# Kernel optimization log

Hardware: AMD Instinct MI355X
Metric: run time of the kernel (lower is better)

Reference implementation:

```python
import jax, jax.numpy as jnp
import numpy as np

B, Hm, Wm, Dm = 1, 32, 32, 32
N = Hm * Wm * Dm
C = 128
HEADS, DH = 8, 16
G = 32
L = 2
OUT = 1


def _ln(x, g, b):
    mu = jnp.mean(x, -1, keepdims=True)
    var = jnp.mean((x - mu) ** 2, -1, keepdims=True)
    return (x - mu) * jax.lax.rsqrt(var + 1e-5) * g + b


def setup_inputs() -> dict:
    key = jax.random.key(0)
    ks = iter(jax.random.split(key, 64))
    def nrm(shape, s=0.02):
        return jax.random.normal(next(ks), shape, jnp.float32) * s
    return {
        "x": jax.random.normal(next(ks), (B, N, 3), jnp.float32),
        "fx": jax.random.normal(next(ks), (B, N, 1), jnp.float32),
        "pre_w1": nrm((4, 2 * C)), "pre_b1": jnp.zeros((2 * C,), jnp.float32),
        "pre_w2": nrm((2 * C, C)), "pre_b2": jnp.zeros((C,), jnp.float32),
        "placeholder": jax.random.uniform(next(ks), (C,), jnp.float32) / C,
        "ln1_g": jnp.ones((L, C), jnp.float32), "ln1_b": jnp.zeros((L, C), jnp.float32),
        "convx_w": nrm((L, C, C, 3, 3, 3)), "convx_b": jnp.zeros((L, C), jnp.float32),
        "convfx_w": nrm((L, C, C, 3, 3, 3)), "convfx_b": jnp.zeros((L, C), jnp.float32),
        "slice_w": nrm((L, DH, G), 0.1), "slice_b": jnp.zeros((L, G), jnp.float32),
        "temperature": jnp.full((L, 1, HEADS, 1, 1), 0.5, jnp.float32),
        "wq": nrm((L, DH, DH), 0.1), "wk": nrm((L, DH, DH), 0.1), "wv": nrm((L, DH, DH), 0.1),
        "wo": nrm((L, HEADS * DH, C)), "bo": jnp.zeros((L, C), jnp.float32),
        "ln2_g": jnp.ones((L, C), jnp.float32), "ln2_b": jnp.zeros((L, C), jnp.float32),
        "mlp_w1": nrm((L, C, C)), "mlp_b1": jnp.zeros((L, C), jnp.float32),
        "mlp_w2": nrm((L, C, C)), "mlp_b2": jnp.zeros((L, C), jnp.float32),
        "ln3_g": jnp.ones((C,), jnp.float32), "ln3_b": jnp.zeros((C,), jnp.float32),
        "out_w": nrm((C, OUT)), "out_b": jnp.zeros((OUT,), jnp.float32),
    }


def _conv3d(x, w, b):
    # x: [B,C,H,W,D], w: [O,I,3,3,3], SAME padding (kernel//2) as torch Conv3d
    y = jax.lax.conv_general_dilated(x, w, (1, 1, 1), "SAME",
                                     dimension_numbers=("NCDHW", "OIDHW", "NCDHW"))
    return y + b[None, :, None, None, None]


def _physics_attn(z, cw_x, cb_x, cw_fx, cb_fx, sw, sb, temp, wq, wk, wv, wo, bo):
    # z: [B, N, C] -> structured mesh conv projections -> slice attention
    xg = z.reshape(B, Hm, Wm, Dm, C).transpose(0, 4, 1, 2, 3)  # [B,C,H,W,D]

    def split_heads(t):  # [B,I,H,W,D] -> [B,heads,N,dh]
        return t.transpose(0, 2, 3, 4, 1).reshape(B, N, HEADS, DH).transpose(0, 2, 1, 3)

    x_mid = split_heads(_conv3d(xg, cw_x, cb_x))
    fx_mid = split_heads(_conv3d(xg, cw_fx, cb_fx))
    # slice assignment weights: [B,heads,N,G], temperature-scaled softmax
    slice_logits = (x_mid @ sw + sb) / temp
    swt = jax.nn.softmax(slice_logits, axis=-1)
    norm = jnp.sum(swt, axis=2)  # [B,heads,G]
    tok = jnp.einsum("bhnc,bhng->bhgc", fx_mid, swt) / (norm + 1e-5)[..., None]
    q, k, v = tok @ wq, tok @ wk, tok @ wv  # [B,heads,G,dh]
    attn = jax.nn.softmax((q @ k.transpose(0, 1, 3, 2)) * (DH ** -0.5), axis=-1)
    ot = attn @ v  # [B,heads,G,dh]
    out = jnp.einsum("bhgc,bhng->bhnc", ot, swt)  # de-slice back to tokens
    out = out.transpose(0, 2, 1, 3).reshape(B, N, HEADS * DH)
    return out @ wo + bo


def reference(x, fx, pre_w1, pre_b1, pre_w2, pre_b2, placeholder,
              ln1_g, ln1_b, convx_w, convx_b, convfx_w, convfx_b,
              slice_w, slice_b, temperature, wq, wk, wv, wo, bo,
              ln2_g, ln2_b, mlp_w1, mlp_b1, mlp_w2, mlp_b2,
              ln3_g, ln3_b, out_w, out_b):
    h = jnp.concatenate([x, fx], axis=-1)  # [B,N,space+fun]
    z = jax.nn.gelu(h @ pre_w1 + pre_b1, approximate=False) @ pre_w2 + pre_b2 + placeholder
    for l in range(L):
        zn = _ln(z, ln1_g[l], ln1_b[l])
        z = _physics_attn(zn, convx_w[l], convx_b[l], convfx_w[l], convfx_b[l],
                          slice_w[l], slice_b[l], temperature[l],
                          wq[l], wk[l], wv[l], wo[l], bo[l]) + z
        zn = _ln(z, ln2_g[l], ln2_b[l])
        z = jax.nn.gelu(zn @ mlp_w1[l] + mlp_b1[l], approximate=False) @ mlp_w2[l] + mlp_b2[l] + z
    return _ln(z, ln3_g, ln3_b) @ out_w + out_b
```

## Files before the change

kernel.cpp:

```cpp
#include <hip/hip_runtime.h>
#include <hip/hip_bf16.h>

#define DEV __device__ __forceinline__

constexpr int N   = 32768;
constexpr int TOTAL_IN = 2038481;

constexpr int OFF_X        = 0;
constexpr int OFF_FX       = 98304;
constexpr int OFF_PRE_W1   = 131072;
constexpr int OFF_PRE_B1   = 132096;
constexpr int OFF_PRE_W2   = 132352;
constexpr int OFF_PRE_B2   = 165120;
constexpr int OFF_PLACE    = 165248;
constexpr int OFF_LN1_G    = 165376;
constexpr int OFF_LN1_B    = 165632;
constexpr int OFF_CONVX_W  = 165888;
constexpr int OFF_CONVX_B  = 1050624;
constexpr int OFF_CONVFX_W = 1050880;
constexpr int OFF_CONVFX_B = 1935616;
constexpr int OFF_SLICE_W  = 1935872;
constexpr int OFF_SLICE_B  = 1936896;
constexpr int OFF_TEMP     = 1936960;
constexpr int OFF_WQ       = 1936976;
constexpr int OFF_WK       = 1937488;
constexpr int OFF_WV       = 1938000;
constexpr int OFF_WO       = 1938512;
constexpr int OFF_BO       = 1971280;
constexpr int OFF_LN2_G    = 1971536;
constexpr int OFF_LN2_B    = 1971792;
constexpr int OFF_MLP_W1   = 1972048;
constexpr int OFF_MLP_B1   = 2004816;
constexpr int OFF_MLP_W2   = 2005072;
constexpr int OFF_MLP_B2   = 2037840;
constexpr int OFF_LN3_G    = 2038096;
constexpr int OFF_LN3_B    = 2038224;
constexpr int OFF_OUT_W    = 2038352;
constexpr int OFF_OUT_B    = 2038480;

__device__ __constant__ int d_PRE[32] = {
  0, 98304, 131072, 132096, 132352, 165120, 165248, 165376, 165632,
  165888, 1050624, 1050880, 1935616, 1935872, 1936896, 1936960, 1936976,
  1937488, 1938000, 1938512, 1971280, 1971536, 1971792, 1972048, 2004816,
  2005072, 2037840, 2038096, 2038224, 2038352, 2038480, 2038481
};

constexpr size_t F_IN   = 16;
constexpr size_t F_WT   = 2038512;
constexpr size_t F_Z    = F_WT   + 1769472;
constexpr size_t F_ZN   = F_Z    + 4194304;
constexpr size_t F_CONV = F_ZN   + 4194304;
constexpr size_t F_SWT  = F_CONV + 8388608;
constexpr size_t F_TOKP = F_SWT  + 8388608;
constexpr size_t F_TOK2 = F_TOKP + 1114112;
constexpr size_t F_WP   = F_TOK2 + 34816;
constexpr size_t F_ZERO = F_WP   + 65536;
constexpr size_t F_END  = F_ZERO + 64;

struct InPtrs { const void* p[31]; };

typedef short short8v  __attribute__((ext_vector_type(8)));
typedef float float4v  __attribute__((ext_vector_type(4)));
#define MFMA16(A,B,C) __builtin_amdgcn_mfma_f32_16x16x32_bf16(A,B,C,0,0,0)

typedef const __attribute__((address_space(1))) void* gas_p;
typedef __attribute__((address_space(3))) void* las_p;

DEV float geluf(float x) { return 0.5f * x * (1.0f + erff(x * 0.70710678118654752f)); }
DEV short f2bs(float x) { union { __hip_bfloat16 h; short s; } c; c.h = __float2bfloat16(x); return c.s; }
DEV float bs2f(short s) { union { unsigned u; float f; } c; c.u = ((unsigned)(unsigned short)s) << 16; return c.f; }

__global__ void k_setup(InPtrs ptrs, float* __restrict__ ws,
                        short* __restrict__ wtf, short* __restrict__ wp) {
  __shared__ short wl[13952];
  const bool isbf = (*(const unsigned*)ptrs.p[15] == 0x3F003F00u);
  int b = blockIdx.x, tid = threadIdx.x;
  if (b < 512) {
    if (b == 0 && tid < 64) ws[F_ZERO + tid] = 0.f;
    int stride = 512 * 256;
    for (int e = b * 256 + tid; e < TOTAL_IN; e += stride) {
      if ((e >= OFF_CONVX_W && e < OFF_CONVX_B) || (e >= OFF_CONVFX_W && e < OFF_CONVFX_B)) continue;
      int lo = 0, hi = 30;
#pragma unroll
      for (int it = 0; it < 5; ++it) {
        int mid = (lo + hi + 1) >> 1;
        if (e >= d_PRE[mid]) lo = mid; else hi = mid - 1;
      }
      int loc = e - d_PRE[lo];
      float v;
      if (isbf) {
        unsigned short u = ((const unsigned short*)ptrs.p[lo])[loc];
        v = __uint_as_float(((unsigned)u) << 16);
      } else {
        v = ((const float*)ptrs.p[lo])[loc];
      }
      ws[F_IN + e] = v;
    }
  } else if (b < 640) {
    int idx = b - 512;
    int layer = idx >> 6, rem = idx & 63;
    int icb = rem >> 4, ntile = rem & 15;
    for (int i = tid; i < 13824; i += 256) {
      int oc_r = i / 864, off = i - oc_r * 864;
      int oc = ntile * 16 + oc_r;
      const void* cw = (oc < 128) ? ptrs.p[9] : ptrs.p[11];
      size_t base = ((size_t)(layer * 128 + (oc & 127)) * 128 + icb * 32) * 27 + off;
      wl[oc_r * 872 + off] = isbf ? (short)((const unsigned short*)cw)[base]
                                  : f2bs(((const float*)cw)[base]);
    }
    __syncthreads();
    int wv = tid >> 6, lane = tid & 63;
    int m = lane & 15, q = lane >> 4;
    for (int tg = 0; tg < 7; ++tg) {
      int tap = tg * 4 + wv;
      if (tap < 27) {
        short8v out;
#pragma unroll
        for (int j = 0; j < 8; ++j) out[j] = wl[m * 872 + (q * 8 + j) * 27 + tap];
        size_t f = ((size_t)((layer * 108 + icb * 27 + tap) * 16 + ntile)) * 64 + lane;
        *(short8v*)(wtf + f * 8) = out;
      }
    }
  } else {
    int f = (b - 640) * 256 + tid;
    int lane = f & 63;
    int t = f >> 6;
    const void* srcb; size_t soff; int kt, nt;
    if (t < 64) { srcb = ptrs.p[4]; soff = 0; kt = t >> 3; nt = t & 7; }
    else {
      int r = t - 64, l = r / 96, r2 = r - l * 96;
      int which = r2 >> 5, idx2 = r2 & 31;
      kt = idx2 >> 3; nt = idx2 & 7;
      srcb = (which == 0 ? ptrs.p[23] : (which == 1 ? ptrs.p[25] : ptrs.p[19]));
      soff = (size_t)l * 16384;
    }
    int k0 = kt * 32 + (lane >> 4) * 8;
    int n = nt * 16 + (lane & 15);
    size_t base = soff + (size_t)k0 * 128 + n;
    short8v out;
    if (isbf) {
      const unsigned short* src = (const unsigned short*)srcb + base;
#pragma unroll
      for (int j = 0; j < 8; ++j) out[j] = (short)src[(size_t)j * 128];
    } else {
      const float* src = (const float*)srcb + base;
#pragma unroll
      for (int j = 0; j < 8; ++j) out[j] = f2bs(src[(size_t)j * 128]);
    }
    *(short8v*)(wp + (size_t)f * 8) = out;
  }
}

__global__ __launch_bounds__(256)
void k_prenet(const float* __restrict__ ip, const short* __restrict__ wp,
              float* __restrict__ z, short* __restrict__ znb) {
  __shared__ float w1s[1024], b1s[256], cvec[128], g1s[128], be1s[128];
  __shared__ float xv[64][4];
  __shared__ __align__(16) short ts[64 * 264];
  int tid = threadIdx.x;
  int wv = tid >> 6, lane = tid & 63;
  int m = lane & 15, q = lane >> 4;
  int n0 = blockIdx.x * 64;
  for (int i = tid; i < 1024; i += 256) w1s[i] = ip[OFF_PRE_W1 + i];
  b1s[tid] = ip[OFF_PRE_B1 + tid];
  if (tid < 128) {
    cvec[tid] = ip[OFF_PRE_B2 + tid] + ip[OFF_PLACE + tid];
    g1s[tid]  = ip[OFF_LN1_G + tid];
    be1s[tid] = ip[OFF_LN1_B + tid];
  }
  if (tid < 64) {
    xv[tid][0] = ip[OFF_X + (n0 + tid) * 3 + 0];
    xv[tid][1] = ip[OFF_X + (n0 + tid) * 3 + 1];
    xv[tid][2] = ip[OFF_X + (n0 + tid) * 3 + 2];
    xv[tid][3] = ip[OFF_FX + n0 + tid];
  }
  __syncthreads();
  {
    float w0 = w1s[tid], wA = w1s[256 + tid], wB = w1s[512 + tid], wC = w1s[768 + tid];
    float bb = b1s[tid];
    for (int t = 0; t < 64; ++t) {
      float hv = bb + xv[t][0] * w0 + xv[t][1] * wA + xv[t][2] * wB + xv[t][3] * wC;
      ts[t * 264 + tid] = f2bs(geluf(hv));
    }
  }
  __syncthreads();
  const short8v* pwf = (const short8v*)wp;
  float4v acc[8];
#pragma unroll
  for (int nt = 0; nt < 8; ++nt) acc[nt] = (float4v){0.f, 0.f, 0.f, 0.f};
  for (int kt = 0; kt < 8; ++kt) {
    short8v A = *(const short8v*)(ts + (wv * 16 + m) * 264 + kt * 32 + q * 8);
#pragma unroll
    for (int nt = 0; nt < 8; ++nt)
      acc[nt] = MFMA16(A, pwf[(kt * 8 + nt) * 64 + lane], acc[nt]);
  }
  float vz[8][4];
#pragma unroll
  for (int nt = 0; nt < 8; ++nt) {
    int col = nt * 16 + m;
#pragma unroll
    for (int r = 0; r < 4; ++r) {
      vz[nt][r] = acc[nt][r] + cvec[col];
      z[(size_t)(n0 + wv * 16 + q * 4 + r) * 128 + col] = vz[nt][r];
    }
  }
#pragma unroll
  for (int r = 0; r < 4; ++r) {
    float s1 = 0.f, s2 = 0.f;
#pragma unroll
    for (int nt = 0; nt < 8; ++nt) { float v = vz[nt][r]; s1 += v; s2 += v * v; }
#pragma unroll
    for (int off = 1; off < 16; off <<= 1) { s1 += __shfl_xor(s1, off); s2 += __shfl_xor(s2, off); }
    float mu = s1 * (1.0f / 128.0f);
    float var = s2 * (1.0f / 128.0f) - mu * mu;
    float rst = 1.0f / sqrtf(var + 1e-5f);
    size_t rowb = (size_t)(n0 + wv * 16 + q * 4 + r) * 128;
#pragma unroll
    for (int nt = 0; nt < 8; ++nt) {
      int col = nt * 16 + m;
      znb[rowb + col] = f2bs((vz[nt][r] - mu) * rst * g1s[col] + be1s[col]);
    }
  }
}

__global__ __launch_bounds__(256)
void k_conv(const float* __restrict__ ip, const short* __restrict__ znb,
            const short* __restrict__ wtf, short* __restrict__ cvb,
            const float* __restrict__ zerof, int layer) {
  __shared__ __align__(16) short halo[26624];
  int tid = threadIdx.x;
  int wv = tid >> 6, lane = tid & 63;
  int m = lane & 15, q = lane >> 4;
  int n0 = blockIdx.x * 64;
  int h = n0 >> 10, w0 = (n0 >> 5) & 31;
  float bias_r[4];
#pragma unroll
  for (int nt = 0; nt < 4; ++nt) {
    int oc = (wv * 4 + nt) * 16 + m;
    bias_r[nt] = (oc < 128) ? ip[OFF_CONVX_B + layer * 128 + oc]
                            : ip[OFF_CONVFX_B + layer * 128 + (oc - 128)];
  }
  float4v acc[4][4];
#pragma unroll
  for (int a = 0; a < 4; ++a)
#pragma unroll
    for (int b = 0; b < 4; ++b) acc[a][b] = (float4v){0.f, 0.f, 0.f, 0.f};

  const short8v* wf = (const short8v*)wtf + (size_t)layer * 110592 + (wv * 4) * 64 + lane;
  short8v bc0 = wf[0], bc1 = wf[64], bc2 = wf[128], bc3 = wf[192];

  auto stage = [&](int icb, short* dst) {
    for (int g = wv; g < 26; g += 4) {
      int c = g * 64 + lane;
      int pr = c >> 2, qq = c & 3;
      int line = pr / 34, dpos = pr - line * 34;
      int hh2 = h + (line >> 2) - 1, ww2 = w0 + (line & 3) - 1, dd2 = dpos - 1;
      bool ok = (pr < 408) && ((unsigned)hh2 < 32u) && ((unsigned)ww2 < 32u) && ((unsigned)dd2 < 32u);
      int tok = (hh2 << 10) + (ww2 << 5) + dd2;
      const void* src = ok ? (const void*)(znb + (size_t)tok * 128 + icb * 32 + qq * 8)
                           : (const void*)zerof;
      __builtin_amdgcn_global_load_lds((gas_p)src, (las_p)(dst + g * 512), 16, 0, 0);
    }
  };

  stage(0, halo);
  __syncthreads();

  int tap = 0, icb = 0;
  for (int kt = 0; kt < 108; ++kt) {
    if (tap == 0 && icb < 3)
      stage(icb + 1, halo + ((icb + 1) & 1) * 13312);
    int ktn = (kt + 1 < 108) ? kt + 1 : kt;
    const short8v* wn = wf + (size_t)ktn * 1024;
    short8v bn0 = wn[0], bn1 = wn[64], bn2 = wn[128], bn3 = wn[192];

    int ta = tap / 9, rem = tap - ta * 9, tb = rem / 3, tc = rem - tb * 3;
    const short* hp = halo + (icb & 1) * 13312 + ((ta * 4 + tb) * 34 + tc + m) * 32 + q * 8;
    short8v A0 = *(const short8v*)(hp);
    short8v A1 = *(const short8v*)(hp + 512);
    short8v A2 = *(const short8v*)(hp + 1088);
    short8v A3 = *(const short8v*)(hp + 1600);

    acc[0][0] = MFMA16(A0, bc0, acc[0][0]);
    acc[1][0] = MFMA16(A1, bc0, acc[1][0]);
    acc[2][0] = MFMA16(A2, bc0, acc[2][0]);
    acc[3][0] = MFMA16(A3, bc0, acc[3][0]);
    acc[0][1] = MFMA16(A0, bc1, acc[0][1]);
    acc[1][1] = MFMA16(A1, bc1, acc[1][1]);
    acc[2][1] = MFMA16(A2, bc1, acc[2][1]);
    acc[3][1] = MFMA16(A3, bc1, acc[3][1]);
    acc[0][2] = MFMA16(A0, bc2, acc[0][2]);
    acc[1][2] = MFMA16(A1, bc2, acc[1][2]);
    acc[2][2] = MFMA16(A2, bc2, acc[2][2]);
    acc[3][2] = MFMA16(A3, bc2, acc[3][2]);
    acc[0][3] = MFMA16(A0, bc3, acc[0][3]);
    acc[1][3] = MFMA16(A1, bc3, acc[1][3]);
    acc[2][3] = MFMA16(A2, bc3, acc[2][3]);
    acc[3][3] = MFMA16(A3, bc3, acc[3][3]);

    bc0 = bn0; bc1 = bn1; bc2 = bn2; bc3 = bn3;
    if (++tap == 27) {
      tap = 0; ++icb;
      __syncthreads();
    }
  }
#pragma unroll
  for (int mt = 0; mt < 4; ++mt) {
    short* cp = cvb + (size_t)(n0 + mt * 16 + q * 4) * 256 + (wv * 4) * 16 + m;
#pragma unroll
    for (int nt = 0; nt < 4; ++nt) {
#pragma unroll
      for (int r = 0; r < 4; ++r)
        cp[(size_t)r * 256 + nt * 16] = f2bs(acc[mt][nt][r] + bias_r[nt]);
    }
  }
}

__global__ __launch_bounds__(256)
void k_slice(const float* __restrict__ ip, const short* __restrict__ cvb,
             short* __restrict__ swtb, float* __restrict__ tokp, int layer) {
  __shared__ float sws[512], sbs[32], its[8];
  __shared__ float swl[32 * 257];
  __shared__ __align__(16) short fxl[32 * 132];
  int tid = threadIdx.x;
  for (int i = tid; i < 512; i += 256) sws[i] = ip[OFF_SLICE_W + layer * 512 + i];
  if (tid < 32) sbs[tid] = ip[OFF_SLICE_B + layer * 32 + tid];
  if (tid < 8)  its[tid] = 1.0f / ip[OFF_TEMP + layer * 8 + tid];
  float4 ta0 = make_float4(0,0,0,0), ta1 = ta0, ta2 = ta0, ta3 = ta0;
  float np = 0.f;
  for (int s = 0; s < 4; ++s) {
    int tbase = blockIdx.x * 128 + s * 32;
    __syncthreads();
    for (int i = tid; i < 512; i += 256) {
      int t = i >> 4, c8 = (i & 15) * 8;
      *(short8v*)(fxl + t * 132 + c8) = *(const short8v*)(cvb + (size_t)(tbase + t) * 256 + 128 + c8);
    }
    {
      int t = tid >> 3, hh = tid & 7;
      float xm[16];
      short8v x0 = *(const short8v*)(cvb + (size_t)(tbase + t) * 256 + hh * 16);
      short8v x1 = *(const short8v*)(cvb + (size_t)(tbase + t) * 256 + hh * 16 + 8);
#pragma unroll
      for (int j = 0; j < 8; ++j) { xm[j] = bs2f(x0[j]); xm[8 + j] = bs2f(x1[j]); }
      float lg[32];
      float itv = its[hh];
#pragma unroll
      for (int g = 0; g < 32; ++g) {
        float sacc = sbs[g];
#pragma unroll
        for (int j = 0; j < 16; ++j) sacc += xm[j] * sws[j * 32 + g];
        lg[g] = sacc * itv;
      }
      float mx = -1e30f;
#pragma unroll
      for (int g = 0; g < 32; ++g) mx = fmaxf(mx, lg[g]);
      float sum = 0.f;
#pragma unroll
      for (int g = 0; g < 32; ++g) { lg[g] = expf(lg[g] - mx); sum += lg[g]; }
      float inv = 1.0f / sum;
#pragma unroll
      for (int g = 0; g < 32; ++g) {
        lg[g] *= inv;
        swl[t * 257 + hh * 32 + g] = lg[g];
      }
#pragma unroll
      for (int qq = 0; qq < 4; ++qq) {
        short8v pk;
#pragma unroll
        for (int j = 0; j < 8; ++j) pk[j] = f2bs(lg[qq * 8 + j]);
        *(short8v*)(swtb + (size_t)(tbase + t) * 256 + hh * 32 + qq * 8) = pk;
      }
    }
    __syncthreads();
    {
      int ah = tid >> 5, ag = tid & 31;
      for (int t2 = 0; t2 < 32; ++t2) {
        float sv = swl[t2 * 257 + ah * 32 + ag];
        np += sv;
        short8v f0 = *(const short8v*)(fxl + t2 * 132 + ah * 16);
        short8v f1 = *(const short8v*)(fxl + t2 * 132 + ah * 16 + 8);
        ta0.x += sv * bs2f(f0[0]); ta0.y += sv * bs2f(f0[1]); ta0.z += sv * bs2f(f0[2]); ta0.w += sv * bs2f(f0[3]);
        ta1.x += sv * bs2f(f0[4]); ta1.y += sv * bs2f(f0[5]); ta1.z += sv * bs2f(f0[6]); ta1.w += sv * bs2f(f0[7]);
        ta2.x += sv * bs2f(f1[0]); ta2.y += sv * bs2f(f1[1]); ta2.z += sv * bs2f(f1[2]); ta2.w += sv * bs2f(f1[3]);
        ta3.x += sv * bs2f(f1[4]); ta3.y += sv * bs2f(f1[5]); ta3.z += sv * bs2f(f1[6]); ta3.w += sv * bs2f(f1[7]);
      }
    }
  }
  int ah = tid >> 5, ag = tid & 31;
  size_t base = (size_t)blockIdx.x * 4352 + (size_t)(ah * 32 + ag) * 16;
  *(float4*)&tokp[base + 0]  = ta0;
  *(float4*)&tokp[base + 4]  = ta1;
  *(float4*)&tokp[base + 8]  = ta2;
  *(float4*)&tokp[base + 12] = ta3;
  tokp[(size_t)blockIdx.x * 4352 + 4096 + ah * 32 + ag] = np;
}

__global__ void k_tokred1(const float* __restrict__ tokp, float* __restrict__ tok2) {
  int ogrp = blockIdx.x % 17, bgrp = blockIdx.x / 17;
  int o = ogrp * 256 + threadIdx.x;
  float s = 0.f;
  int b0 = bgrp * 32;
#pragma unroll 8
  for (int b = b0; b < b0 + 32; ++b) s += tokp[(size_t)b * 4352 + o];
  tok2[(size_t)bgrp * 4352 + o] = s;
}

__global__ __launch_bounds__(256)
void k_fused(const float* __restrict__ ip, const short* __restrict__ swtb,
             const float* __restrict__ tok2, const short* __restrict__ wp,
             float* __restrict__ z, short* __restrict__ znb,
             void* __restrict__ dout, const void* __restrict__ tempraw, int layer) {
  __shared__ __align__(16) char smem[64512];
  short* otb = (short*)smem;
  float* bia = (float*)(smem + 8192);
  float* trs = (float*)(smem + 12288);
  short* znt = (short*)(smem + 12288);
  float* kk  = (float*)(smem + 29696);
  short* al  = (short*)(smem + 29696);
  float* vvs = (float*)(smem + 47104);
  float* bol = bia, *b1s = bia + 128, *b2s = bia + 256, *g2s = bia + 384;
  float* be2s = bia + 512, *lng = bia + 640, *lnb = bia + 768, *ows = bia + 896;
  int tid = threadIdx.x;
  int wv = tid >> 6, lane = tid & 63;
  int m = lane & 15, q = lane >> 4;
  int n0 = blockIdx.x * 64;
  if (tid < 128) {
    bol[tid]  = ip[OFF_BO + layer * 128 + tid];
    b1s[tid]  = ip[OFF_MLP_B1 + layer * 128 + tid];
    b2s[tid]  = ip[OFF_MLP_B2 + layer * 128 + tid];
    g2s[tid]  = ip[OFF_LN2_G + layer * 128 + tid];
    be2s[tid] = ip[OFF_LN2_B + layer * 128 + tid];
    if (layer == 0) {
      lng[tid] = ip[OFF_LN1_G + 128 + tid];
      lnb[tid] = ip[OFF_LN1_B + 128 + tid];
      ows[tid] = 0.f;
    } else {
      lng[tid] = ip[OFF_LN3_G + tid];
      lnb[tid] = ip[OFF_LN3_B + tid];
      ows[tid] = ip[OFF_OUT_W + tid];
    }
  }
  for (int i = tid; i < 4352; i += 256) {
    float s = 0.f;
#pragma unroll
    for (int b = 0; b < 8; ++b) s += tok2[(size_t)b * 4352 + i];
    trs[i] = s;
  }
  __syncthreads();
  float qv[16];
  {
    const float* wqp = ip + OFF_WQ + layer * 256;
    const float* wkp = ip + OFF_WK + layer * 256;
    const float* wvp = ip + OFF_WV + layer * 256;
    float inv = 1.0f / (trs[4096 + tid] + 1e-5f);
    float t[16];
#pragma unroll
    for (int c = 0; c < 16; ++c) t[c] = trs[tid * 16 + c] * inv;
#pragma unroll
    for (int c = 0; c < 16; ++c) {
      float aq = 0.f, ak = 0.f, av = 0.f;
#pragma unroll
      for (int j = 0; j < 16; ++j) {
        float tv = t[j];
        aq += tv * wqp[j * 16 + c];
        ak += tv * wkp[j * 16 + c];
        av += tv * wvp[j * 16 + c];
      }
      qv[c] = aq;
      kk[tid * 17 + c] = ak;
      vvs[tid * 17 + c] = av;
    }
  }
  __syncthreads();
  {
    int hh = tid >> 5, g = tid & 31;
    float sc[32];
    float mx = -1e30f;
#pragma unroll
    for (int g2 = 0; g2 < 32; ++g2) {
      float s = 0.f;
#pragma unroll
      for (int c = 0; c < 16; ++c) s += qv[c] * kk[(hh * 32 + g2) * 17 + c];
      s *= 0.25f;
      sc[g2] = s; mx = fmaxf(mx, s);
    }
    float sum = 0.f;
#pragma unroll
    for (int g2 = 0; g2 < 32; ++g2) { sc[g2] = expf(sc[g2] - mx); sum += sc[g2]; }
    float inv2 = 1.0f / sum;
    float o[16];
#pragma unroll
    for (int c = 0; c < 16; ++c) o[c] = 0.f;
#pragma unroll
    for (int g2 = 0; g2 < 32; ++g2) {
      float p = sc[g2] * inv2;
#pragma unroll
      for (int c = 0; c < 16; ++c) o[c] += p * vvs[(hh * 32 + g2) * 17 + c];
    }
#pragma unroll
    for (int dh = 0; dh < 16; ++dh)
      otb[hh * 512 + (((g >> 3) * 16 + dh) << 3) + (g & 7)] = f2bs(o[dh]);
  }
  __syncthreads();
  float4v accd[8];
#pragma unroll
  for (int h = 0; h < 8; ++h) accd[h] = (float4v){0.f, 0.f, 0.f, 0.f};
#pragma unroll
  for (int h = 0; h < 8; ++h) {
    short8v A = *(const short8v*)(swtb + (size_t)(n0 + wv * 16 + m) * 256 + h * 32 + q * 8);
    accd[h] = MFMA16(A, *(const short8v*)(otb + h * 512 + lane * 8), accd[h]);
  }
  __syncthreads();
#pragma unroll
  for (int h = 0; h < 8; ++h)
#pragma unroll
    for (int r = 0; r < 4; ++r)
      al[(wv * 16 + q * 4 + r) * 136 + h * 16 + m] = f2bs(accd[h][r]);
  __syncthreads();
  const short8v* wof = (const short8v*)(wp + (size_t)(128 + 96 * layer) * 512);
  float4v a2[8];
#pragma unroll
  for (int nt = 0; nt < 8; ++nt) a2[nt] = (float4v){0.f, 0.f, 0.f, 0.f};
  for (int kt = 0; kt < 4; ++kt) {
    short8v A = *(const short8v*)(al + (wv * 16 + m) * 136 + kt * 32 + q * 8);
#pragma unroll
    for (int nt = 0; nt < 8; ++nt)
      a2[nt] = MFMA16(A, wof[(kt * 8 + nt) * 64 + lane], a2[nt]);
  }
  float vmid[8][4];
#pragma unroll
  for (int nt = 0; nt < 8; ++nt) {
    int col = nt * 16 + m;
#pragma unroll
    for (int r = 0; r < 4; ++r)
      vmid[nt][r] = z[(size_t)(n0 + wv * 16 + q * 4 + r) * 128 + col] + a2[nt][r] + bol[col];
  }
#pragma unroll
  for (int r = 0; r < 4; ++r) {
    float s1 = 0.f, s2 = 0.f;
#pragma unroll
    for (int nt = 0; nt < 8; ++nt) { float v = vmid[nt][r]; s1 += v; s2 += v * v; }
#pragma unroll
    for (int off = 1; off < 16; off <<= 1) { s1 += __shfl_xor(s1, off); s2 += __shfl_xor(s2, off); }
    float mu = s1 * (1.0f / 128.0f);
    float var = s2 * (1.0f / 128.0f) - mu * mu;
    float rst = 1.0f / sqrtf(var + 1e-5f);
#pragma unroll
    for (int nt = 0; nt < 8; ++nt) {
      int col = nt * 16 + m;
      znt[(wv * 16 + q * 4 + r) * 136 + col] = f2bs((vmid[nt][r] - mu) * rst * g2s[col] + be2s[col]);
    }
  }
  __syncthreads();
  const short8v* w1f = (const short8v*)(wp + (size_t)(64 + 96 * layer) * 512);
  const short8v* w2f = (const short8v*)(wp + (size_t)(96 + 96 * layer) * 512);
  float4v acc[8];
#pragma unroll
  for (int nt = 0; nt < 8; ++nt) acc[nt] = (float4v){0.f, 0.f, 0.f, 0.f};
  for (int kt = 0; kt < 4; ++kt) {
    short8v A = *(const short8v*)(znt + (wv * 16 + m) * 136 + kt * 32 + q * 8);
#pragma unroll
    for (int nt = 0; nt < 8; ++nt)
      acc[nt] = MFMA16(A, w1f[(kt * 8 + nt) * 64 + lane], acc[nt]);
  }
  __syncthreads();
#pragma unroll
  for (int nt = 0; nt < 8; ++nt) {
    int col = nt * 16 + m;
#pragma unroll
    for (int r = 0; r < 4; ++r)
      al[(wv * 16 + q * 4 + r) * 136 + col] = f2bs(geluf(acc[nt][r] + b1s[col]));
  }
  __syncthreads();
  float4v a4[8];
#pragma unroll
  for (int nt = 0; nt < 8; ++nt) a4[nt] = (float4v){0.f, 0.f, 0.f, 0.f};
  for (int kt = 0; kt < 4; ++kt) {
    short8v A = *(const short8v*)(al + (wv * 16 + m) * 136 + kt * 32 + q * 8);
#pragma unroll
    for (int nt = 0; nt < 8; ++nt)
      a4[nt] = MFMA16(A, w2f[(kt * 8 + nt) * 64 + lane], a4[nt]);
  }
  float vfin[8][4];
#pragma unroll
  for (int nt = 0; nt < 8; ++nt) {
    int col = nt * 16 + m;
#pragma unroll
    for (int r = 0; r < 4; ++r) {
      vfin[nt][r] = vmid[nt][r] + a4[nt][r] + b2s[col];
      z[(size_t)(n0 + wv * 16 + q * 4 + r) * 128 + col] = vfin[nt][r];
    }
  }
#pragma unroll
  for (int r = 0; r < 4; ++r) {
    float s1 = 0.f, s2 = 0.f;
#pragma unroll
    for (int nt = 0; nt < 8; ++nt) { float v = vfin[nt][r]; s1 += v; s2 += v * v; }
#pragma unroll
    for (int off = 1; off < 16; off <<= 1) { s1 += __shfl_xor(s1, off); s2 += __shfl_xor(s2, off); }
    float mu = s1 * (1.0f / 128.0f);
    float var = s2 * (1.0f / 128.0f) - mu * mu;
    float rst = 1.0f / sqrtf(var + 1e-5f);
    int n = n0 + wv * 16 + q * 4 + r;
    if (layer == 0) {
      size_t rowb = (size_t)n * 128;
#pragma unroll
      for (int nt = 0; nt < 8; ++nt) {
        int col = nt * 16 + m;
        znb[rowb + col] = f2bs((vfin[nt][r] - mu) * rst * lng[col] + lnb[col]);
      }
    } else {
      float contrib = 0.f;
#pragma unroll
      for (int nt = 0; nt < 8; ++nt) {
        int col = nt * 16 + m;
        contrib += ((vfin[nt][r] - mu) * rst * lng[col] + lnb[col]) * ows[col];
      }
#pragma unroll
      for (int off = 1; off < 16; off <<= 1) contrib += __shfl_xor(contrib, off);
      if (m == 0) {
        float res = contrib + ip[OFF_OUT_B];
        unsigned tw = *(const unsigned*)tempraw;
        if (tw == 0x3F003F00u) ((__hip_bfloat16*)dout)[n] = __float2bfloat16(res);
        else                   ((float*)dout)[n] = res;
      }
    }
  }
}

extern "C" void kernel_launch(void* const* d_in, const int* in_sizes, int n_in,
                              void* d_out, int out_size, void* d_ws, size_t ws_size,
                              hipStream_t stream) {
  (void)in_sizes; (void)out_size; (void)ws_size;
  if (n_in < 31) return;
  float* ws   = (float*)d_ws;
  float* ip   = ws + F_IN;
  short* wtf  = (short*)(ws + F_WT);
  float* z    = ws + F_Z;
  short* znb  = (short*)(ws + F_ZN);
  short* cvb  = (short*)(ws + F_CONV);
  short* swtb = (short*)(ws + F_SWT);
  float* tkp  = ws + F_TOKP;
  float* tk2  = ws + F_TOK2;
  short* wp   = (short*)(ws + F_WP);
  float* zf   = ws + F_ZERO;

  InPtrs P;
  for (int i = 0; i < 31; ++i) P.p[i] = d_in[i];

  k_setup <<<704, 256, 0, stream>>>(P, ws, wtf, wp);
  k_prenet<<<512, 256, 0, stream>>>(ip, wp, z, znb);
  for (int l = 0; l < 2; ++l) {
    k_conv   <<<512, 256, 0, stream>>>(ip, znb, wtf, cvb, zf, l);
    k_slice  <<<256, 256, 0, stream>>>(ip, cvb, swtb, tkp, l);
    k_tokred1<<<136, 256, 0, stream>>>(tkp, tk2);
    k_fused  <<<512, 256, 0, stream>>>(ip, swtb, tk2, wp, z, znb, d_out, d_in[15], l);
  }
}
```

Measured before the change: 443.6 us.

## Single-buffer conv halo in LDS with padded per-quad layout, trim setup grid

The conv kernel drops the double-buffered async global_load_lds halo staging. It now loads each input-channel block synchronously through registers into one smaller LDS buffer, with a quad-major padded layout that changes the A-fragment read strides, presumably to cut bank conflicts. Out-of-range halo points are written as zeros in registers, so the global zero buffer is gone. The setup kernel iterates only over non-conv-weight elements with fewer blocks. Halving LDS may allow more resident blocks, but the halo load no longer overlaps with MFMA work.

Result: slower. 478.6 us (+7.9%).

```diff
diff --git a/kernel.cpp b/kernel.cpp
--- a/kernel.cpp
+++ b/kernel.cpp
@@ -45,6 +45,10 @@
   2005072, 2037840, 2038096, 2038224, 2038352, 2038480, 2038481
 };
 
+constexpr int CVT_A = 165888;
+constexpr int CVT_B = CVT_A + 256;
+constexpr int CVT_TOTAL = CVT_B + (TOTAL_IN - OFF_CONVFX_B);
+
 constexpr size_t F_IN   = 16;
 constexpr size_t F_WT   = 2038512;
 constexpr size_t F_Z    = F_WT   + 1769472;
@@ -54,17 +58,13 @@
 constexpr size_t F_TOKP = F_SWT  + 8388608;
 constexpr size_t F_TOK2 = F_TOKP + 1114112;
 constexpr size_t F_WP   = F_TOK2 + 34816;
-constexpr size_t F_ZERO = F_WP   + 65536;
-constexpr size_t F_END  = F_ZERO + 64;
+constexpr size_t F_END  = F_WP   + 65536;
 
 struct InPtrs { const void* p[31]; };
 
 typedef short short8v  __attribute__((ext_vector_type(8)));
 typedef float float4v  __attribute__((ext_vector_type(4)));
 #define MFMA16(A,B,C) __builtin_amdgcn_mfma_f32_16x16x32_bf16(A,B,C,0,0,0)
-
-typedef const __attribute__((address_space(1))) void* gas_p;
-typedef __attribute__((address_space(3))) void* las_p;
 
 DEV float geluf(float x) { return 0.5f * x * (1.0f + erff(x * 0.70710678118654752f)); }
 DEV short f2bs(float x) { union { __hip_bfloat16 h; short s; } c; c.h = __float2bfloat16(x); return c.s; }
@@ -75,11 +75,12 @@
   __shared__ short wl[13952];
   const bool isbf = (*(const unsigned*)ptrs.p[15] == 0x3F003F00u);
   int b = blockIdx.x, tid = threadIdx.x;
-  if (b < 512) {
-    if (b == 0 && tid < 64) ws[F_ZERO + tid] = 0.f;
-    int stride = 512 * 256;
-    for (int e = b * 256 + tid; e < TOTAL_IN; e += stride) {
-      if ((e >= OFF_CONVX_W && e < OFF_CONVX_B) || (e >= OFF_CONVFX_W && e < OFF_CONVFX_B)) continue;
+  if (b < 128) {
+    int stride = 128 * 256;
+    for (int idx = b * 256 + tid; idx < CVT_TOTAL; idx += stride) {
+      int e = (idx < CVT_A) ? idx
+            : (idx < CVT_B) ? (OFF_CONVX_B + (idx - CVT_A))
+                            : (OFF_CONVFX_B + (idx - CVT_B));
       int lo = 0, hi = 30;
 #pragma unroll
       for (int it = 0; it < 5; ++it) {
@@ -96,8 +97,8 @@
       }
       ws[F_IN + e] = v;
     }
-  } else if (b < 640) {
-    int idx = b - 512;
+  } else if (b < 256) {
+    int idx = b - 128;
     int layer = idx >> 6, rem = idx & 63;
     int icb = rem >> 4, ntile = rem & 15;
     for (int i = tid; i < 13824; i += 256) {
@@ -122,7 +123,7 @@
       }
     }
   } else {
-    int f = (b - 640) * 256 + tid;
+    int f = (b - 256) * 256 + tid;
     int lane = f & 63;
     int t = f >> 6;
     const void* srcb; size_t soff; int kt, nt;
@@ -225,9 +226,8 @@
 
 __global__ __launch_bounds__(256)
 void k_conv(const float* __restrict__ ip, const short* __restrict__ znb,
-            const short* __restrict__ wtf, short* __restrict__ cvb,
-            const float* __restrict__ zerof, int layer) {
-  __shared__ __align__(16) short halo[26624];
+            const short* __restrict__ wtf, short* __restrict__ cvb, int layer) {
+  __shared__ __align__(16) short halo[15360];
   int tid = threadIdx.x;
   int wv = tid >> 6, lane = tid & 63;
   int m = lane & 15, q = lane >> 4;
@@ -249,37 +249,33 @@
   const short8v* wf = (const short8v*)wtf + (size_t)layer * 110592 + (wv * 4) * 64 + lane;
   short8v bc0 = wf[0], bc1 = wf[64], bc2 = wf[128], bc3 = wf[192];
 
-  auto stage = [&](int icb, short* dst) {
-    for (int g = wv; g < 26; g += 4) {
-      int c = g * 64 + lane;
-      int pr = c >> 2, qq = c & 3;
-      int line = pr / 34, dpos = pr - line * 34;
-      int hh2 = h + (line >> 2) - 1, ww2 = w0 + (line & 3) - 1, dd2 = dpos - 1;
-      bool ok = (pr < 408) && ((unsigned)hh2 < 32u) && ((unsigned)ww2 < 32u) && ((unsigned)dd2 < 32u);
-      int tok = (hh2 << 10) + (ww2 << 5) + dd2;
-      const void* src = ok ? (const void*)(znb + (size_t)tok * 128 + icb * 32 + qq * 8)
-                           : (const void*)zerof;
-      __builtin_amdgcn_global_load_lds((gas_p)src, (las_p)(dst + g * 512), 16, 0, 0);
-    }
-  };
-
-  stage(0, halo);
-  __syncthreads();
-
   int tap = 0, icb = 0;
   for (int kt = 0; kt < 108; ++kt) {
-    if (tap == 0 && icb < 3)
-      stage(icb + 1, halo + ((icb + 1) & 1) * 13312);
+    if (tap == 0) {
+      __syncthreads();
+      for (int i = tid; i < 1632; i += 256) {
+        int pr = i >> 2, qq = i & 3;
+        int line = pr / 34, dpos = pr - line * 34;
+        int hh2 = h + (line >> 2) - 1, ww2 = w0 + (line & 3) - 1, dd2 = dpos - 1;
+        short8v v = (short8v){0, 0, 0, 0, 0, 0, 0, 0};
+        if (((unsigned)hh2 < 32u) && ((unsigned)ww2 < 32u) && ((unsigned)dd2 < 32u)) {
+          int tok = (hh2 << 10) + (ww2 << 5) + dd2;
+          v = *(const short8v*)(znb + (size_t)tok * 128 + icb * 32 + qq * 8);
+        }
+        *(short8v*)(halo + qq * 3840 + (line * 40 + dpos) * 8) = v;
+      }
+      __syncthreads();
+    }
     int ktn = (kt + 1 < 108) ? kt + 1 : kt;
     const short8v* wn = wf + (size_t)ktn * 1024;
     short8v bn0 = wn[0], bn1 = wn[64], bn2 = wn[128], bn3 = wn[192];
 
     int ta = tap / 9, rem = tap - ta * 9, tb = rem / 3, tc = rem - tb * 3;
-    const short* hp = halo + (icb & 1) * 13312 + ((ta * 4 + tb) * 34 + tc + m) * 32 + q * 8;
+    const short* hp = halo + q * 3840 + ((ta * 4 + tb) * 40 + tc + m) * 8;
     short8v A0 = *(const short8v*)(hp);
-    short8v A1 = *(const short8v*)(hp + 512);
-    short8v A2 = *(const short8v*)(hp + 1088);
-    short8v A3 = *(const short8v*)(hp + 1600);
+    short8v A1 = *(const short8v*)(hp + 128);
+    short8v A2 = *(const short8v*)(hp + 320);
+    short8v A3 = *(const short8v*)(hp + 448);
 
     acc[0][0] = MFMA16(A0, bc0, acc[0][0]);
     acc[1][0] = MFMA16(A1, bc0, acc[1][0]);
@@ -299,10 +295,7 @@
     acc[3][3] = MFMA16(A3, bc3, acc[3][3]);
 
     bc0 = bn0; bc1 = bn1; bc2 = bn2; bc3 = bn3;
-    if (++tap == 27) {
-      tap = 0; ++icb;
-      __syncthreads();
-    }
+    if (++tap == 27) { tap = 0; ++icb; }
   }
 #pragma unroll
   for (int mt = 0; mt < 4; ++mt) {
@@ -643,15 +636,14 @@
   float* tkp  = ws + F_TOKP;
   float* tk2  = ws + F_TOK2;
   short* wp   = (short*)(ws + F_WP);
-  float* zf   = ws + F_ZERO;
 
   InPtrs P;
   for (int i = 0; i < 31; ++i) P.p[i] = d_in[i];
 
-  k_setup <<<704, 256, 0, stream>>>(P, ws, wtf, wp);
+  k_setup <<<320, 256, 0, stream>>>(P, ws, wtf, wp);
   k_prenet<<<512, 256, 0, stream>>>(ip, wp, z, znb);
   for (int l = 0; l < 2; ++l) {
-    k_conv   <<<512, 256, 0, stream>>>(ip, znb, wtf, cvb, zf, l);
+    k_conv   <<<512, 256, 0, stream>>>(ip, znb, wtf, cvb, l);
     k_slice  <<<256, 256, 0, stream>>>(ip, cvb, swtb, tkp, l);
     k_tokred1<<<136, 256, 0, stream>>>(tkp, tk2);
     k_fused  <<<512, 256, 0, stream>>>(ip, swtb, tk2, wp, z, znb, d_out, d_in[15], l);
```
